# Optimization experiments

Measured on AMD Instinct MI355X. Metric: run time of the kernel, lower is better.

The kernel has to match this reference:

```python
import jax, jax.numpy as jnp
import numpy as np

B, NUM, LENTH, AUX = 32, 64, 64, 64
SIZE, OUT = 256, 256
IN_G = (LENTH + 1) * 2 + AUX  # 194


def _linear_params(k, fan_in, fan_out):
    # torch nn.Linear default init: U(-1/sqrt(fan_in), 1/sqrt(fan_in))
    s = 1.0 / np.sqrt(fan_in)
    kw, kb = jax.random.split(k)
    W = jax.random.uniform(kw, (fan_in, fan_out), minval=-s, maxval=s, dtype=jnp.float32)
    b = jax.random.uniform(kb, (fan_out,), minval=-s, maxval=s, dtype=jnp.float32)
    return W, b


def setup_inputs() -> dict:
    key = jax.random.key(0)
    ks = jax.random.split(key, 8)
    inp = {"x_aux": jax.random.normal(ks[0], (B, NUM, LENTH + AUX), dtype=jnp.float32)}
    dims = [("g1", IN_G, SIZE), ("g2", SIZE, SIZE), ("g3", SIZE, SIZE), ("g4", SIZE, OUT),
            ("f1", OUT, SIZE), ("f2", SIZE, SIZE), ("f3", SIZE, OUT)]
    for k, (name, fi, fo) in zip(ks[1:], dims):
        W, b = _linear_params(k, fi, fo)
        inp[name + "_w"] = W
        inp[name + "_b"] = b
    return inp


def reference(x_aux, g1_w, g1_b, g2_w, g2_b, g3_w, g3_b, g4_w, g4_b,
              f1_w, f1_b, f2_w, f2_b, f3_w, f3_b):
    bsz = x_aux.shape[0]
    # coord feature = object index i
    coord = jnp.broadcast_to(
        jnp.arange(NUM, dtype=x_aux.dtype)[None, :, None], (bsz, NUM, 1))
    x = jnp.concatenate([x_aux[:, :, :LENTH], coord], axis=-1)      # [B, N, LENTH+1]
    xa = jnp.concatenate([x_aux, coord], axis=-1)                   # [B, N, LENTH+AUX+1]
    # all-pairs broadcast+concat -> [B, N, N, IN_G]
    x_i = jnp.broadcast_to(x[:, None, :, :], (bsz, NUM, NUM, LENTH + 1))
    x_j = jnp.broadcast_to(xa[:, :, None, :], (bsz, NUM, NUM, LENTH + AUX + 1))
    pairs = jnp.concatenate([x_i, x_j], axis=-1)
    # shared g-MLP over every pair
    h = jax.nn.relu(pairs @ g1_w + g1_b)
    h = jax.nn.relu(h @ g2_w + g2_b)
    h = jax.nn.relu(h @ g3_w + g3_b)
    h = jax.nn.relu(h @ g4_w + g4_b)
    # sum-pool over all N*N pairs -> [B, OUT]
    x_g = h.sum(axis=(1, 2))
    # f-MLP (dropout treated as identity / eval mode)
    x_f = jax.nn.relu(x_g @ f1_w + f1_b)
    x_f = jax.nn.relu(x_f @ f2_w + f2_b)
    return x_f @ f3_w + f3_b
```

## Files before the change

### kernel.cpp

```cpp
#include <hip/hip_runtime.h>

#define BATCH 32
#define NOBJ  64
#define PADK  264

typedef _Float16 f16x2 __attribute__((ext_vector_type(2)));
typedef __fp16   h16x2 __attribute__((ext_vector_type(2)));
typedef _Float16 f16x4 __attribute__((ext_vector_type(4)));
typedef _Float16 f16x8 __attribute__((ext_vector_type(8)));
typedef float    f32x4 __attribute__((ext_vector_type(4)));
typedef float    f32x16 __attribute__((ext_vector_type(16)));

#define MFMA32(a, b, c) __builtin_amdgcn_mfma_f32_32x32x16_f16((a), (b), (c), 0, 0, 0)


__global__ __launch_bounds__(256) void prep_all(
    const float* __restrict__ x_aux,
    const float* __restrict__ g1w, const float* __restrict__ g1b,
    const float* __restrict__ g2w, const float* __restrict__ g3w,
    const float* __restrict__ g4w,
    _Float16* __restrict__ wtf, float* __restrict__ xg,
    float* __restrict__ cib, float* __restrict__ h0j) {
  __shared__ __align__(16) _Float16 tile[256][33];
  const int blk = blockIdx.x;
  const int t = threadIdx.x;

  if (blk < 32) {
    xg[blk * 256 + t] = 0.0f;
    const int l = blk >> 3;
    if (l == 0) return;
    const int nt = blk & 7;
    const float* src = (l == 1) ? g2w : (l == 2) ? g3w : g4w;

    const int nn = t & 31, kb = t >> 5;
#pragma unroll 4
    for (int pass = 0; pass < 32; ++pass) {
      int kp = pass * 8 + kb;
      tile[kp][nn] = (_Float16)src[(size_t)kp * 256 + nt * 32 + nn];
    }
    __syncthreads();

    const int lane = t & 63;
    const int nfrag = lane & 31;
    const int kbase = (lane >> 5) * 8;
    _Float16* dst = wtf + ((size_t)(l * 8 + nt) * 16) * 512;
#pragma unroll
    for (int q = 0; q < 4; ++q) {
      int kk = (t >> 6) + 4 * q;
      f16x8 fr;
#pragma unroll
      for (int j = 0; j < 8; ++j)
        fr[j] = tile[kk * 16 + kbase + j][nfrag];
      *(f16x8*)(dst + (size_t)kk * 512 + lane * 8) = fr;
    }
  } else if (blk < 544) {
    float* xs = (float*)&tile[0][0];
    const int blkc = blk - 32;
    const int b  = blkc >> 4;
    const int i0 = (blkc & 15) * 4;

#pragma unroll
    for (int u = 0; u < 2; ++u) {
      int idx = u * 256 + t;
      int j = idx >> 7, k = idx & 127;
      xs[j * 128 + k] = x_aux[((size_t)(b * NOBJ + i0 + j)) * 128 + k];
    }
    __syncthreads();

    float c0 = 0.f, c1 = 0.f, c2 = 0.f, c3 = 0.f;
#pragma unroll 2
    for (int k = 0; k < 128; k += 4) {
      f32x4 x0 = *(const f32x4*)&xs[k];
      f32x4 x1 = *(const f32x4*)&xs[128 + k];
      f32x4 x2 = *(const f32x4*)&xs[256 + k];
      f32x4 x3 = *(const f32x4*)&xs[384 + k];
#pragma unroll
      for (int q = 0; q < 4; ++q) {
        float w = g1w[(size_t)(65 + k + q) * 256 + t];
        c0 += x0[q] * w; c1 += x1[q] * w;
        c2 += x2[q] * w; c3 += x3[q] * w;
      }
    }
    float wc = g1w[(size_t)193 * 256 + t];
    float bb = g1b[t];
    c0 += (float)(i0 + 0) * wc + bb;
    c1 += (float)(i0 + 1) * wc + bb;
    c2 += (float)(i0 + 2) * wc + bb;
    c3 += (float)(i0 + 3) * wc + bb;
    cib[((size_t)(b * NOBJ + i0 + 0)) * 256 + t] = c0;
    cib[((size_t)(b * NOBJ + i0 + 1)) * 256 + t] = c1;
    cib[((size_t)(b * NOBJ + i0 + 2)) * 256 + t] = c2;
    cib[((size_t)(b * NOBJ + i0 + 3)) * 256 + t] = c3;
  } else {
    float* xs = (float*)&tile[0][0];
    const int blk2 = blk - 544;
    const int b  = blk2 >> 3;
    const int j0 = (blk2 & 7) * 8;

#pragma unroll
    for (int u = 0; u < 2; ++u) {
      int idx = u * 256 + t;
      int jj = idx >> 6, k = idx & 63;
      xs[jj * 68 + k] = x_aux[((size_t)(b * NOBJ + j0 + jj)) * 128 + k];
    }
    __syncthreads();

    float acc[8] = {};
#pragma unroll 2
    for (int k = 0; k < 64; k += 4) {
      f32x4 xv[8];
#pragma unroll
      for (int jj = 0; jj < 8; ++jj)
        xv[jj] = *(const f32x4*)&xs[jj * 68 + k];
#pragma unroll
      for (int q = 0; q < 4; ++q) {
        float w = g1w[(size_t)(k + q) * 256 + t];
#pragma unroll
        for (int jj = 0; jj < 8; ++jj) acc[jj] += xv[jj][q] * w;
      }
    }
    float wc = g1w[(size_t)64 * 256 + t];
#pragma unroll
    for (int jj = 0; jj < 8; ++jj)
      h0j[((size_t)(b * NOBJ + j0 + jj)) * 256 + t] =
          acc[jj] + (float)(j0 + jj) * wc;
  }
}

__device__ __forceinline__ void layer16(
    const _Float16* __restrict__ bp0, const _Float16* __restrict__ bp1,
    const _Float16* __restrict__ arow,
    f16x8 pb00, f16x8 pb01, f16x8 pb10, f16x8 pb11,
    f32x16 acc[4]) {
  __builtin_amdgcn_s_setprio(1);
#pragma unroll
  for (int kk = 0; kk < 16; ++kk) {
    f16x8 b0 = (kk == 0) ? pb00 : (kk == 1) ? pb10
               : *(const f16x8*)(bp0 + (size_t)kk * 512);
    f16x8 b1 = (kk == 0) ? pb01 : (kk == 1) ? pb11
               : *(const f16x8*)(bp1 + (size_t)kk * 512);
    f16x8 a0 = *(const f16x8*)(arow + (size_t)kk * 16);
    f16x8 a1 = *(const f16x8*)(arow + (size_t)32 * PADK + kk * 16);
    acc[0] = MFMA32(a0, b0, acc[0]);
    acc[1] = MFMA32(a0, b1, acc[1]);
    acc[2] = MFMA32(a1, b0, acc[2]);
    acc[3] = MFMA32(a1, b1, acc[3]);
  }
  __builtin_amdgcn_s_setprio(0);
}

__global__ __launch_bounds__(512, 4) void g_mlp_pool(
    const float* __restrict__ h0j,
    const float* __restrict__ cib,
    const _Float16* __restrict__ wtf,
    const float* __restrict__ g2b, const float* __restrict__ g3b,
    const float* __restrict__ g4b,
    float* __restrict__ xg) {
  __shared__ __align__(16) _Float16 As[128][PADK];

  const int b  = blockIdx.x >> 5;
  const int i0 = (blockIdx.x & 31) * 2;
  const int t  = threadIdx.x;
  const int lane = t & 63;
  const int wv   = t >> 6;

  const int nq   = wv & 3;
  const int mh   = wv >> 2;
  const int c31  = lane & 31;
  const int h    = lane >> 5;
  const int n0   = nq * 64;

  const _Float16* b1p0 = wtf + ((size_t)(1 * 8 + nq * 2) * 16) * 512 + lane * 8;
  const _Float16* b1p1 = b1p0 + 16 * 512;
  const _Float16* b2p0 = wtf + ((size_t)(2 * 8 + nq * 2) * 16) * 512 + lane * 8;
  const _Float16* b2p1 = b2p0 + 16 * 512;
  const _Float16* b3p0 = wtf + ((size_t)(3 * 8 + nq * 2) * 16) * 512 + lane * 8;
  const _Float16* b3p1 = b3p0 + 16 * 512;

  {
    const int c = lane * 4;
    const float* hb = h0j + (size_t)(b * NOBJ) * 256 + c;
    const float* c0p = cib + (size_t)(b * NOBJ + i0) * 256 + c;
    f32x4 cv0 = *(const f32x4*)c0p;
    f32x4 cv1 = *(const f32x4*)(c0p + 256);
#pragma unroll
    for (int it = 0; it < 8; ++it) {
      int j = it * 8 + wv;
      f32x4 hv = *(const f32x4*)(hb + (size_t)j * 256);
      f16x4 p0, p1;
#pragma unroll
      for (int q = 0; q < 4; ++q) {
        p0[q] = (_Float16)fmaxf(hv[q] + cv0[q], 0.f);
        p1[q] = (_Float16)fmaxf(hv[q] + cv1[q], 0.f);
      }
      *(f16x4*)&As[j][c]      = p0;
      *(f16x4*)&As[64 + j][c] = p1;
    }
  }

  f16x8 pb00 = *(const f16x8*)(b1p0);
  f16x8 pb01 = *(const f16x8*)(b1p1);
  f16x8 pb10 = *(const f16x8*)(b1p0 + 512);
  f16x8 pb11 = *(const f16x8*)(b1p1 + 512);
  __syncthreads();

  const _Float16* arow = &As[c31][h * 8] + (size_t)mh * 64 * PADK;
  const float bv20 = g2b[n0 + c31], bv21 = g2b[n0 + 32 + c31];
  const float bv30 = g3b[n0 + c31], bv31 = g3b[n0 + 32 + c31];
  const float bv40 = g4b[n0 + c31], bv41 = g4b[n0 + 32 + c31];

  f32x16 acc[4];

#pragma unroll
  for (int x = 0; x < 4; ++x) acc[x] = (f32x16){};
  layer16(b1p0, b1p1, arow, pb00, pb01, pb10, pb11, acc);

  pb00 = *(const f16x8*)(b2p0);
  pb01 = *(const f16x8*)(b2p1);
  pb10 = *(const f16x8*)(b2p0 + 512);
  pb11 = *(const f16x8*)(b2p1 + 512);
  __syncthreads();
#pragma unroll
  for (int m = 0; m < 2; ++m)
#pragma unroll
    for (int g = 0; g < 4; ++g)
#pragma unroll
      for (int r = 0; r < 4; ++r) {
        const int row = (mh * 2 + m) * 32 + g * 8 + h * 4 + r;
        const int reg = g * 4 + r;
        As[row][n0 + c31]      = (_Float16)fmaxf(acc[m * 2][reg] + bv20, 0.f);
        As[row][n0 + 32 + c31] = (_Float16)fmaxf(acc[m * 2 + 1][reg] + bv21, 0.f);
      }
  __syncthreads();

#pragma unroll
  for (int x = 0; x < 4; ++x) acc[x] = (f32x16){};
  layer16(b2p0, b2p1, arow, pb00, pb01, pb10, pb11, acc);

  pb00 = *(const f16x8*)(b3p0);
  pb01 = *(const f16x8*)(b3p1);
  pb10 = *(const f16x8*)(b3p0 + 512);
  pb11 = *(const f16x8*)(b3p1 + 512);
  __syncthreads();
#pragma unroll
  for (int m = 0; m < 2; ++m)
#pragma unroll
    for (int g = 0; g < 4; ++g)
#pragma unroll
      for (int r = 0; r < 4; ++r) {
        const int row = (mh * 2 + m) * 32 + g * 8 + h * 4 + r;
        const int reg = g * 4 + r;
        As[row][n0 + c31]      = (_Float16)fmaxf(acc[m * 2][reg] + bv30, 0.f);
        As[row][n0 + 32 + c31] = (_Float16)fmaxf(acc[m * 2 + 1][reg] + bv31, 0.f);
      }
  __syncthreads();

#pragma unroll
  for (int x = 0; x < 4; ++x) acc[x] = (f32x16){};
  layer16(b3p0, b3p1, arow, pb00, pb01, pb10, pb11, acc);

  float s0 = 0.f, s1 = 0.f;
#pragma unroll
  for (int m = 0; m < 2; ++m)
#pragma unroll
    for (int reg = 0; reg < 16; ++reg) {
      s0 += fmaxf(acc[m * 2][reg] + bv40, 0.f);
      s1 += fmaxf(acc[m * 2 + 1][reg] + bv41, 0.f);
    }
  s0 += __shfl_xor(s0, 32, 64);
  s1 += __shfl_xor(s1, 32, 64);
  if (h == 0) {
    atomicAdd(&xg[b * 256 + n0 + c31], s0);
    atomicAdd(&xg[b * 256 + n0 + 32 + c31], s1);
  }
}

__global__ __launch_bounds__(1024) void f_mlp(
    const float* __restrict__ xg,
    const float* __restrict__ f1w, const float* __restrict__ f1b,
    const float* __restrict__ f2w, const float* __restrict__ f2b,
    const float* __restrict__ f3w, const float* __restrict__ f3b,
    float* __restrict__ out) {
  __shared__ float xs[256], ys[256], ps[4][256];
  const int b = blockIdx.x;
  const int t = threadIdx.x;
  const int n = t & 255;
  const int kc = t >> 8;

  if (t < 256) xs[t] = xg[b * 256 + t];
  __syncthreads();

  float p = 0.f;
#pragma unroll 8
  for (int k0 = 0; k0 < 64; ++k0) {
    int k = kc * 64 + k0;
    p += xs[k] * f1w[k * 256 + n];
  }
  ps[kc][n] = p;
  __syncthreads();
  if (t < 256)
    ys[t] = fmaxf(f1b[t] + ps[0][t] + ps[1][t] + ps[2][t] + ps[3][t], 0.f);
  __syncthreads();

  p = 0.f;
#pragma unroll 8
  for (int k0 = 0; k0 < 64; ++k0) {
    int k = kc * 64 + k0;
    p += ys[k] * f2w[k * 256 + n];
  }
  ps[kc][n] = p;
  __syncthreads();
  if (t < 256)
    xs[t] = fmaxf(f2b[t] + ps[0][t] + ps[1][t] + ps[2][t] + ps[3][t], 0.f);
  __syncthreads();

  p = 0.f;
#pragma unroll 8
  for (int k0 = 0; k0 < 64; ++k0) {
    int k = kc * 64 + k0;
    p += xs[k] * f3w[k * 256 + n];
  }
  ps[kc][n] = p;
  __syncthreads();
  if (t < 256)
    out[b * 256 + t] = f3b[t] + ps[0][t] + ps[1][t] + ps[2][t] + ps[3][t];
}

extern "C" void kernel_launch(void* const* d_in, const int* in_sizes, int n_in,
                              void* d_out, int out_size, void* d_ws, size_t ws_size,
                              hipStream_t stream) {
  const float* x_aux = (const float*)d_in[0];
  const float* g1w = (const float*)d_in[1];
  const float* g1b = (const float*)d_in[2];
  const float* g2w = (const float*)d_in[3];
  const float* g2b = (const float*)d_in[4];
  const float* g3w = (const float*)d_in[5];
  const float* g3b = (const float*)d_in[6];
  const float* g4w = (const float*)d_in[7];
  const float* g4b = (const float*)d_in[8];
  const float* f1w = (const float*)d_in[9];
  const float* f1b = (const float*)d_in[10];
  const float* f2w = (const float*)d_in[11];
  const float* f2b = (const float*)d_in[12];
  const float* f3w = (const float*)d_in[13];
  const float* f3b = (const float*)d_in[14];
  float* out = (float*)d_out;

  _Float16* wtf = (_Float16*)d_ws;
  float* xg  = (float*)((char*)d_ws + 512u * 1024u);
  float* cib = (float*)((char*)d_ws + 544u * 1024u);
  float* h0j = (float*)((char*)d_ws + 544u * 1024u + 2048u * 1024u);

  hipLaunchKernelGGL(prep_all, dim3(800), dim3(256), 0, stream,
                     x_aux, g1w, g1b, g2w, g3w, g4w, wtf, xg, cib, h0j);
  hipLaunchKernelGGL(g_mlp_pool, dim3(BATCH * 32), dim3(512), 0, stream,
                     h0j, cib, wtf, g2b, g3b, g4b, xg);
  hipLaunchKernelGGL(f_mlp, dim3(BATCH), dim3(1024), 0, stream,
                     xg, f1w, f1b, f2w, f2b, f3w, f3b, out);
}
```

Measured before the change: 154.1 us.

## Shrink g-MLP blocks to one object row and software-pipeline weight loads

Each block of the fused g-MLP now handles a single i-row (64 pairs) with 4 waves instead of two rows with 8 waves, so the grid doubles and LDS per block halves. The weight fragments are held in a 4-deep register ring and prefetched 4 k-steps ahead. The next layer's first fragments are loaded during the tail of the current layer. The s_setprio hints are removed. This aims to hide global weight-load latency and raise occupancy. In exchange, weights are re-read by twice as many blocks and each wave uses more registers.

```diff
diff --git a/kernel.cpp b/kernel.cpp
--- a/kernel.cpp
+++ b/kernel.cpp
@@ -127,84 +127,80 @@
   }
 }
 
-__device__ __forceinline__ void layer16(
+template <bool PRELOAD_NEXT>
+__device__ __forceinline__ void layer_run(
     const _Float16* __restrict__ bp0, const _Float16* __restrict__ bp1,
+    const _Float16* __restrict__ bn0, const _Float16* __restrict__ bn1,
     const _Float16* __restrict__ arow,
-    f16x8 pb00, f16x8 pb01, f16x8 pb10, f16x8 pb11,
-    f32x16 acc[4]) {
-  __builtin_amdgcn_s_setprio(1);
+    f16x8 (&u0)[4], f16x8 (&u1)[4], f32x16 (&acc)[4]) {
 #pragma unroll
   for (int kk = 0; kk < 16; ++kk) {
-    f16x8 b0 = (kk == 0) ? pb00 : (kk == 1) ? pb10
-               : *(const f16x8*)(bp0 + (size_t)kk * 512);
-    f16x8 b1 = (kk == 0) ? pb01 : (kk == 1) ? pb11
-               : *(const f16x8*)(bp1 + (size_t)kk * 512);
+    f16x8 b0 = u0[kk & 3];
+    f16x8 b1 = u1[kk & 3];
     f16x8 a0 = *(const f16x8*)(arow + (size_t)kk * 16);
     f16x8 a1 = *(const f16x8*)(arow + (size_t)32 * PADK + kk * 16);
     acc[0] = MFMA32(a0, b0, acc[0]);
     acc[1] = MFMA32(a0, b1, acc[1]);
     acc[2] = MFMA32(a1, b0, acc[2]);
     acc[3] = MFMA32(a1, b1, acc[3]);
-  }
-  __builtin_amdgcn_s_setprio(0);
-}
-
-__global__ __launch_bounds__(512, 4) void g_mlp_pool(
+    if (kk < 12) {
+      u0[kk & 3] = *(const f16x8*)(bp0 + (size_t)(kk + 4) * 512);
+      u1[kk & 3] = *(const f16x8*)(bp1 + (size_t)(kk + 4) * 512);
+    } else if (PRELOAD_NEXT) {
+      u0[kk & 3] = *(const f16x8*)(bn0 + (size_t)(kk - 12) * 512);
+      u1[kk & 3] = *(const f16x8*)(bn1 + (size_t)(kk - 12) * 512);
+    }
+  }
+}
+
+__global__ __launch_bounds__(256, 4) void g_mlp_pool(
     const float* __restrict__ h0j,
     const float* __restrict__ cib,
     const _Float16* __restrict__ wtf,
     const float* __restrict__ g2b, const float* __restrict__ g3b,
     const float* __restrict__ g4b,
     float* __restrict__ xg) {
-  __shared__ __align__(16) _Float16 As[128][PADK];
-
-  const int b  = blockIdx.x >> 5;
-  const int i0 = (blockIdx.x & 31) * 2;
+  __shared__ __align__(16) _Float16 As[64][PADK];
+
+  const int b  = blockIdx.x >> 6;
+  const int i0 = blockIdx.x & 63;
   const int t  = threadIdx.x;
   const int lane = t & 63;
   const int wv   = t >> 6;
 
-  const int nq   = wv & 3;
-  const int mh   = wv >> 2;
   const int c31  = lane & 31;
   const int h    = lane >> 5;
-  const int n0   = nq * 64;
-
-  const _Float16* b1p0 = wtf + ((size_t)(1 * 8 + nq * 2) * 16) * 512 + lane * 8;
-  const _Float16* b1p1 = b1p0 + 16 * 512;
-  const _Float16* b2p0 = wtf + ((size_t)(2 * 8 + nq * 2) * 16) * 512 + lane * 8;
-  const _Float16* b2p1 = b2p0 + 16 * 512;
-  const _Float16* b3p0 = wtf + ((size_t)(3 * 8 + nq * 2) * 16) * 512 + lane * 8;
-  const _Float16* b3p1 = b3p0 + 16 * 512;
+  const int n0   = wv * 64;
+
+  const _Float16* L1 = wtf + ((size_t)(8  + 2 * wv) * 16) * 512 + lane * 8;
+  const _Float16* L2 = wtf + ((size_t)(16 + 2 * wv) * 16) * 512 + lane * 8;
+  const _Float16* L3 = wtf + ((size_t)(24 + 2 * wv) * 16) * 512 + lane * 8;
+
+  f16x8 u0[4], u1[4];
+#pragma unroll
+  for (int q = 0; q < 4; ++q) {
+    u0[q] = *(const f16x8*)(L1 + (size_t)q * 512);
+    u1[q] = *(const f16x8*)(L1 + 16 * 512 + (size_t)q * 512);
+  }
 
   {
     const int c = lane * 4;
     const float* hb = h0j + (size_t)(b * NOBJ) * 256 + c;
-    const float* c0p = cib + (size_t)(b * NOBJ + i0) * 256 + c;
-    f32x4 cv0 = *(const f32x4*)c0p;
-    f32x4 cv1 = *(const f32x4*)(c0p + 256);
-#pragma unroll
-    for (int it = 0; it < 8; ++it) {
-      int j = it * 8 + wv;
+    f32x4 cv = *(const f32x4*)(cib + (size_t)(b * NOBJ + i0) * 256 + c);
+#pragma unroll
+    for (int it = 0; it < 16; ++it) {
+      int j = it * 4 + wv;
       f32x4 hv = *(const f32x4*)(hb + (size_t)j * 256);
-      f16x4 p0, p1;
-#pragma unroll
-      for (int q = 0; q < 4; ++q) {
-        p0[q] = (_Float16)fmaxf(hv[q] + cv0[q], 0.f);
-        p1[q] = (_Float16)fmaxf(hv[q] + cv1[q], 0.f);
-      }
-      *(f16x4*)&As[j][c]      = p0;
-      *(f16x4*)&As[64 + j][c] = p1;
-    }
-  }
-
-  f16x8 pb00 = *(const f16x8*)(b1p0);
-  f16x8 pb01 = *(const f16x8*)(b1p1);
-  f16x8 pb10 = *(const f16x8*)(b1p0 + 512);
-  f16x8 pb11 = *(const f16x8*)(b1p1 + 512);
-  __syncthreads();
-
-  const _Float16* arow = &As[c31][h * 8] + (size_t)mh * 64 * PADK;
+      f16x4 p;
+#pragma unroll
+      for (int q = 0; q < 4; ++q)
+        p[q] = (_Float16)fmaxf(hv[q] + cv[q], 0.f);
+      *(f16x4*)&As[j][c] = p;
+    }
+  }
+  __syncthreads();
+
+  const _Float16* arow = &As[c31][h * 8];
   const float bv20 = g2b[n0 + c31], bv21 = g2b[n0 + 32 + c31];
   const float bv30 = g3b[n0 + c31], bv31 = g3b[n0 + 32 + c31];
   const float bv40 = g4b[n0 + c31], bv41 = g4b[n0 + 32 + c31];
@@ -213,12 +209,8 @@
 
 #pragma unroll
   for (int x = 0; x < 4; ++x) acc[x] = (f32x16){};
-  layer16(b1p0, b1p1, arow, pb00, pb01, pb10, pb11, acc);
-
-  pb00 = *(const f16x8*)(b2p0);
-  pb01 = *(const f16x8*)(b2p1);
-  pb10 = *(const f16x8*)(b2p0 + 512);
-  pb11 = *(const f16x8*)(b2p1 + 512);
+  layer_run<true>(L1, L1 + 16 * 512, L2, L2 + 16 * 512, arow, u0, u1, acc);
+
   __syncthreads();
 #pragma unroll
   for (int m = 0; m < 2; ++m)
@@ -226,7 +218,7 @@
     for (int g = 0; g < 4; ++g)
 #pragma unroll
       for (int r = 0; r < 4; ++r) {
-        const int row = (mh * 2 + m) * 32 + g * 8 + h * 4 + r;
+        const int row = m * 32 + g * 8 + h * 4 + r;
         const int reg = g * 4 + r;
         As[row][n0 + c31]      = (_Float16)fmaxf(acc[m * 2][reg] + bv20, 0.f);
         As[row][n0 + 32 + c31] = (_Float16)fmaxf(acc[m * 2 + 1][reg] + bv21, 0.f);
@@ -235,12 +227,8 @@
 
 #pragma unroll
   for (int x = 0; x < 4; ++x) acc[x] = (f32x16){};
-  layer16(b2p0, b2p1, arow, pb00, pb01, pb10, pb11, acc);
-
-  pb00 = *(const f16x8*)(b3p0);
-  pb01 = *(const f16x8*)(b3p1);
-  pb10 = *(const f16x8*)(b3p0 + 512);
-  pb11 = *(const f16x8*)(b3p1 + 512);
+  layer_run<true>(L2, L2 + 16 * 512, L3, L3 + 16 * 512, arow, u0, u1, acc);
+
   __syncthreads();
 #pragma unroll
   for (int m = 0; m < 2; ++m)
@@ -248,7 +236,7 @@
     for (int g = 0; g < 4; ++g)
 #pragma unroll
       for (int r = 0; r < 4; ++r) {
-        const int row = (mh * 2 + m) * 32 + g * 8 + h * 4 + r;
+        const int row = m * 32 + g * 8 + h * 4 + r;
         const int reg = g * 4 + r;
         As[row][n0 + c31]      = (_Float16)fmaxf(acc[m * 2][reg] + bv30, 0.f);
         As[row][n0 + 32 + c31] = (_Float16)fmaxf(acc[m * 2 + 1][reg] + bv31, 0.f);
@@ -257,7 +245,7 @@
 
 #pragma unroll
   for (int x = 0; x < 4; ++x) acc[x] = (f32x16){};
-  layer16(b3p0, b3p1, arow, pb00, pb01, pb10, pb11, acc);
+  layer_run<false>(L3, L3 + 16 * 512, nullptr, nullptr, arow, u0, u1, acc);
 
   float s0 = 0.f, s1 = 0.f;
 #pragma unroll
@@ -353,7 +341,7 @@
 
   hipLaunchKernelGGL(prep_all, dim3(800), dim3(256), 0, stream,
                      x_aux, g1w, g1b, g2w, g3w, g4w, wtf, xg, cib, h0j);
-  hipLaunchKernelGGL(g_mlp_pool, dim3(BATCH * 32), dim3(512), 0, stream,
+  hipLaunchKernelGGL(g_mlp_pool, dim3(BATCH * NOBJ), dim3(256), 0, stream,
                      h0j, cib, wtf, g2b, g3b, g4b, xg);
   hipLaunchKernelGGL(f_mlp, dim3(BATCH), dim3(1024), 0, stream,
                      xg, f1w, f1b, f2w, f2b, f3w, f3b, out);
```

Result: no change. 154.8 us (+0.5%).
